# Kernel optimization log

Measured on AMD Instinct MI355X. Metric: run time of the kernel, lower is better.

The kernel has to match this reference:

```python
import jax, jax.numpy as jnp
import numpy as np

N_NODES = 50000
N_EDGES = 800000
D_FEAT = 128      # node feature dim (== coef_dim)
COEF_DIM = 128
OUT_DIM = 128     # node_layer / neighbour_layer output dim
EPS = 1e-12       # tf.math.l2_normalize epsilon


def setup_inputs() -> dict:
    key = jax.random.key(0)
    ks = jax.random.split(key, 8)
    s = 1.0 / np.sqrt(D_FEAT)
    h = jax.random.normal(ks[0], (N_NODES, D_FEAT), dtype=jnp.float32)
    src = jax.random.randint(ks[1], (N_EDGES,), 0, N_NODES, dtype=jnp.int32)
    dst = jax.random.randint(ks[2], (N_EDGES,), 0, N_NODES, dtype=jnp.int32)
    W_coef = jax.random.normal(ks[3], (D_FEAT, COEF_DIM), dtype=jnp.float32) * s
    b_coef = jnp.zeros((COEF_DIM,), dtype=jnp.float32)
    W_red = jax.random.normal(ks[4], (2 * COEF_DIM, 1), dtype=jnp.float32) * (1.0 / np.sqrt(2 * COEF_DIM))
    b_red = jnp.zeros((1,), dtype=jnp.float32)
    W_node = jax.random.normal(ks[5], (D_FEAT, OUT_DIM), dtype=jnp.float32) * s
    b_node = jnp.zeros((OUT_DIM,), dtype=jnp.float32)
    W_neigh = jax.random.normal(ks[6], (D_FEAT, OUT_DIM), dtype=jnp.float32) * s
    b_neigh = jnp.zeros((OUT_DIM,), dtype=jnp.float32)
    return {"h": h, "src": src, "dst": dst,
            "W_coef": W_coef, "b_coef": b_coef,
            "W_red": W_red, "b_red": b_red,
            "W_node": W_node, "b_node": b_node,
            "W_neigh": W_neigh, "b_neigh": b_neigh}


def reference(h, src, dst, W_coef, b_coef, W_red, b_red, W_node, b_node, W_neigh, b_neigh):
    n = h.shape[0]
    # message func: per-edge coef transform of source features (activation=None)
    q = h @ W_coef + b_coef                      # [N, C] dst-side coef features
    m = q[src]                                   # [E, C] (coef_layer(h[src]))
    # reduce func: attention score per edge from concat(dst coef, message)
    e = jnp.concatenate([q[dst], m], axis=-1) @ W_red + b_red   # [E, 1]
    e = e[:, 0]
    # softmax over incoming edges of each destination node (stable)
    emax = jax.ops.segment_max(e, dst, num_segments=n)          # [N]
    ex = jnp.exp(e - emax[dst])                                 # [E]
    denom = jax.ops.segment_sum(ex, dst, num_segments=n)        # [N]
    alpha = ex / (denom[dst] + EPS)                             # [E]
    # weighted neighbour aggregation of raw source features ('neigh' mailbox)
    agg = jax.ops.segment_sum(alpha[:, None] * h[src], dst, num_segments=n)  # [N, D]
    # new_h = concat(node_layer(h), neighbour_layer(agg))
    new_h = jnp.concatenate([h @ W_node + b_node, agg @ W_neigh + b_neigh], axis=-1)  # [N, 2*OUT]
    # tf.math.l2_normalize along last axis
    sq = jnp.sum(new_h * new_h, axis=-1, keepdims=True)
    return new_h * jax.lax.rsqrt(jnp.maximum(sq, EPS))
```

## Files before the change

### kernel.cpp

```cpp
#include <hip/hip_runtime.h>
#include <hip/hip_bf16.h>
#include <math.h>

#define N_NODES 50000
#define N_EDGES 800000
#define D_FEAT  128
#define EPSF    1e-12f

#define NPG     120
#define NG      417
#define CHUNK_E 4096
#define NCHUNK  196
#define GCAP    2560

#define OFF_U2      0
#define OFF_GCUR    1024
#define OFF_ES      4096
#define OFF_ROWPTR  204800
#define OFF_WTN     405504
#define OFF_WTG     438272
#define OFF_SSRCW   471040
#define OFF_HB      6871040
#define OFF_BUCKET  19671040

typedef __attribute__((ext_vector_type(8))) short bf8;
typedef __attribute__((ext_vector_type(4))) float f4;

__global__ void make_u2_kernel(const float* __restrict__ W_coef,
                               const float* __restrict__ W_red,
                               float* __restrict__ u2, int* __restrict__ gcursor) {
    __shared__ float wr[128];
    int k = threadIdx.x;
    wr[k] = W_red[128 + k];
    for (int i = k; i < NG; i += 128) gcursor[i] = 0;
    __syncthreads();
    const float4* row = (const float4*)(W_coef + k * 128);
    float acc = 0.f;
    #pragma unroll
    for (int j = 0; j < 32; ++j) {
        float4 v = row[j];
        acc += v.x * wr[4*j] + v.y * wr[4*j+1] + v.z * wr[4*j+2] + v.w * wr[4*j+3];
    }
    u2[k] = acc;
}

__global__ __launch_bounds__(256) void prep_kernel(
        const float* __restrict__ h, const float* __restrict__ u2,
        const float* __restrict__ Wn, const float* __restrict__ Wg,
        const int* __restrict__ src, const int* __restrict__ dst,
        float* __restrict__ es, unsigned short* __restrict__ hb,
        unsigned short* __restrict__ WtN, unsigned short* __restrict__ WtG,
        int* __restrict__ gcursor, int* __restrict__ bucket) {
    int b = blockIdx.x;
    if (b < 12500) {
        int node = b * 4 + (threadIdx.x >> 6);
        int lane = threadIdx.x & 63;
        float2 hv = ((const float2*)(h + (size_t)node * 128))[lane];
        float2 uv = ((const float2*)u2)[lane];
        float v = hv.x * uv.x + hv.y * uv.y;
        #pragma unroll
        for (int off = 32; off; off >>= 1) v += __shfl_xor(v, off);
        if (lane == 0) es[node] = __expf(v);
        __hip_bfloat162 p = __float22bfloat162_rn(hv);
        ((unsigned int*)(hb + (size_t)node * 128))[lane] = *(unsigned int*)&p;
    } else if (b < 12564) {
        int idx = (b - 12500) * 256 + threadIdx.x;
        int n = idx >> 7, k = idx & 127;
        __hip_bfloat16 a = __float2bfloat16(Wn[k * 128 + n]);
        __hip_bfloat16 g = __float2bfloat16(Wg[k * 128 + n]);
        WtN[n * 128 + k] = *(unsigned short*)&a;
        WtG[n * 128 + k] = *(unsigned short*)&g;
    } else {
        __shared__ int lh[NG];
        __shared__ int base[NG];
        __shared__ int cnt2[NG];
        int chunk = b - 12564;
        int tid = threadIdx.x;
        for (int i = tid; i < NG; i += 256) { lh[i] = 0; cnt2[i] = 0; }
        __syncthreads();
        int base_e = chunk * CHUNK_E;
        #pragma unroll
        for (int it = 0; it < CHUNK_E / 256; ++it) {
            int e = base_e + it * 256 + tid;
            if (e < N_EDGES) atomicAdd(&lh[(unsigned)dst[e] / NPG], 1);
        }
        __syncthreads();
        for (int i = tid; i < NG; i += 256) {
            int c = lh[i];
            base[i] = c ? atomicAdd(&gcursor[i], c) : 0;
        }
        __syncthreads();
        #pragma unroll
        for (int it = 0; it < CHUNK_E / 256; ++it) {
            int e = base_e + it * 256 + tid;
            if (e < N_EDGES) {
                int d = dst[e];
                int g = (unsigned)d / NPG;
                int r = atomicAdd(&cnt2[g], 1);
                int p = base[g] + r;
                if (p < GCAP)
                    bucket[(size_t)g * GCAP + p] = src[e] | ((d - g * NPG) << 16);
            }
        }
    }
}

__global__ __launch_bounds__(128) void fine_kernel(
        const int* __restrict__ gcnt, const int* __restrict__ bucket,
        const float* __restrict__ es,
        int* __restrict__ row_ptr, int2* __restrict__ ssrc_w) {
    __shared__ int cnt[NPG];
    __shared__ int cnt2[NPG];
    __shared__ int sexcl[NPG];
    __shared__ int ws[2];
    __shared__ int red[2];
    int g = blockIdx.x, tid = threadIdx.x;
    int lane = tid & 63, wid = tid >> 6;

    int partial = 0;
    for (int i = tid; i < g; i += 128) partial += gcnt[i];
    #pragma unroll
    for (int off = 32; off; off >>= 1) partial += __shfl_down(partial, off);
    if (lane == 0) red[wid] = partial;
    if (tid < NPG) { cnt[tid] = 0; cnt2[tid] = 0; }
    __syncthreads();
    int beg = red[0] + red[1];
    int cnt_g = min(gcnt[g], GCAP);
    const int* bk = bucket + (size_t)g * GCAP;

    for (int i = tid; i < cnt_g; i += 128)
        atomicAdd(&cnt[bk[i] >> 16], 1);
    __syncthreads();
    int v = (tid < NPG) ? cnt[tid] : 0;
    int incl = v;
    #pragma unroll
    for (int off = 1; off < 64; off <<= 1) {
        int t = __shfl_up(incl, off);
        if (lane >= off) incl += t;
    }
    if (lane == 63) ws[wid] = incl;
    __syncthreads();
    if (wid == 1) incl += ws[0];
    int excl = incl - v;
    if (tid < NPG) sexcl[tid] = excl;
    int node = g * NPG + tid;
    if (tid < NPG && node < N_NODES) row_ptr[node] = beg + excl;
    if (g == NG - 1 && tid == 0) row_ptr[N_NODES] = N_EDGES;
    __syncthreads();
    for (int i = tid; i < cnt_g; i += 128) {
        int p = bk[i];
        int loc = p >> 16;
        int sv = p & 0xFFFF;
        float wv = es[sv];
        int r = atomicAdd(&cnt2[loc], 1);
        ssrc_w[beg + sexcl[loc] + r] = make_int2(sv, __float_as_int(wv));
    }
}

__global__ __launch_bounds__(512) void agg_gemm_kernel(
        const int* __restrict__ row_ptr, const int2* __restrict__ ssrc_w,
        const unsigned short* __restrict__ hb,
        const unsigned short* __restrict__ WtN, const unsigned short* __restrict__ WtG,
        const float* __restrict__ b_node, const float* __restrict__ b_neigh,
        float* __restrict__ out) {
    __shared__ __align__(16) unsigned short aggt[32][136];
    __shared__ float ssrp[8][16];
    int tid = threadIdx.x;
    int wave = tid >> 6, lane = tid & 63;
    int node0 = blockIdx.x * 32;
    int q = lane >> 4, l16 = lane & 15;

    {
        int g32 = tid >> 4;
        int node = node0 + g32;
        int beg = 0, deg = 0;
        if (node < N_NODES) {
            beg = row_ptr[node];
            deg = row_ptr[node + 1] - beg;
        }
        float acc[8] = {0.f, 0.f, 0.f, 0.f, 0.f, 0.f, 0.f, 0.f};
        float wsum = 0.f;
        #pragma unroll 4
        for (int i = 0; i < deg; ++i) {
            int2 pw = ssrc_w[beg + i];
            float wv = __int_as_float(pw.y);
            wsum += wv;
            uint4 hv = *(const uint4*)(hb + (size_t)pw.x * 128 + l16 * 8);
            acc[0] = fmaf(wv, __uint_as_float(hv.x << 16),        acc[0]);
            acc[1] = fmaf(wv, __uint_as_float(hv.x & 0xFFFF0000u), acc[1]);
            acc[2] = fmaf(wv, __uint_as_float(hv.y << 16),        acc[2]);
            acc[3] = fmaf(wv, __uint_as_float(hv.y & 0xFFFF0000u), acc[3]);
            acc[4] = fmaf(wv, __uint_as_float(hv.z << 16),        acc[4]);
            acc[5] = fmaf(wv, __uint_as_float(hv.z & 0xFFFF0000u), acc[5]);
            acc[6] = fmaf(wv, __uint_as_float(hv.w << 16),        acc[6]);
            acc[7] = fmaf(wv, __uint_as_float(hv.w & 0xFFFF0000u), acc[7]);
        }
        float inv = 1.f / (wsum + EPSF);
        unsigned o[4];
        #pragma unroll
        for (int j = 0; j < 4; ++j) {
            __hip_bfloat162 p = __float22bfloat162_rn(
                make_float2(acc[2*j] * inv, acc[2*j+1] * inv));
            o[j] = *(unsigned*)&p;
        }
        *(uint4*)&aggt[g32][l16 * 8] = make_uint4(o[0], o[1], o[2], o[3]);
    }
    __syncthreads();

    int rt = wave & 1, tq = wave >> 1;
    int half = tq >> 1, tb = (tq & 1) * 4;
    const unsigned short* Wt = half ? WtG : WtN;
    size_t arow = (size_t)min(node0 + rt * 16 + l16, N_NODES - 1);

    f4 acc[4];
    #pragma unroll
    for (int tt = 0; tt < 4; ++tt) acc[tt] = (f4){0.f, 0.f, 0.f, 0.f};
    #pragma unroll
    for (int kc = 0; kc < 4; ++kc) {
        int kbase = kc * 32 + q * 8;
        bf8 a = half ? *(const bf8*)&aggt[rt * 16 + l16][kbase]
                     : *(const bf8*)(hb + arow * 128 + kbase);
        #pragma unroll
        for (int tt = 0; tt < 4; ++tt) {
            int t = tb + tt;
            bf8 bb = *(const bf8*)(Wt + (size_t)(t * 16 + l16) * 128 + kbase);
            acc[tt] = __builtin_amdgcn_mfma_f32_16x16x32_bf16(a, bb, acc[tt], 0, 0, 0);
        }
    }

    float ssr[4] = {0.f, 0.f, 0.f, 0.f};
    #pragma unroll
    for (int tt = 0; tt < 4; ++tt) {
        int t = tb + tt;
        float bv = (half ? b_neigh : b_node)[t * 16 + l16];
        #pragma unroll
        for (int r = 0; r < 4; ++r) {
            acc[tt][r] += bv;
            ssr[r] = fmaf(acc[tt][r], acc[tt][r], ssr[r]);
        }
    }
    #pragma unroll
    for (int r = 0; r < 4; ++r) {
        ssr[r] += __shfl_xor(ssr[r], 1);
        ssr[r] += __shfl_xor(ssr[r], 2);
        ssr[r] += __shfl_xor(ssr[r], 4);
        ssr[r] += __shfl_xor(ssr[r], 8);
    }
    if (l16 == 0) {
        #pragma unroll
        for (int r = 0; r < 4; ++r) ssrp[wave][q * 4 + r] = ssr[r];
    }
    __syncthreads();
    #pragma unroll
    for (int r = 0; r < 4; ++r) {
        int row = q * 4 + r;
        float tot = ssrp[rt][row] + ssrp[rt + 2][row] +
                    ssrp[rt + 4][row] + ssrp[rt + 6][row];
        float sc = rsqrtf(fmaxf(tot, EPSF));
        int node = node0 + rt * 16 + row;
        if (node < N_NODES) {
            float* o = out + (size_t)node * 256 + half * 128;
            #pragma unroll
            for (int tt = 0; tt < 4; ++tt)
                o[(tb + tt) * 16 + l16] = acc[tt][r] * sc;
        }
    }
}

extern "C" void kernel_launch(void* const* d_in, const int* in_sizes, int n_in,
                              void* d_out, int out_size, void* d_ws, size_t ws_size,
                              hipStream_t stream) {
    const float* h       = (const float*)d_in[0];
    const int*   src     = (const int*)d_in[1];
    const int*   dst     = (const int*)d_in[2];
    const float* W_coef  = (const float*)d_in[3];
    const float* W_red   = (const float*)d_in[5];
    const float* W_node  = (const float*)d_in[7];
    const float* b_node  = (const float*)d_in[8];
    const float* W_neigh = (const float*)d_in[9];
    const float* b_neigh = (const float*)d_in[10];
    float* out = (float*)d_out;

    char* w = (char*)d_ws;
    float*          u2      = (float*)(w + OFF_U2);
    int*            gcursor = (int*)(w + OFF_GCUR);
    float*          es      = (float*)(w + OFF_ES);
    int*            row_ptr = (int*)(w + OFF_ROWPTR);
    unsigned short* WtN     = (unsigned short*)(w + OFF_WTN);
    unsigned short* WtG     = (unsigned short*)(w + OFF_WTG);
    int2*           ssrc_w  = (int2*)(w + OFF_SSRCW);
    unsigned short* hb      = (unsigned short*)(w + OFF_HB);
    int*            bucket  = (int*)(w + OFF_BUCKET);

    make_u2_kernel<<<1, 128, 0, stream>>>(W_coef, W_red, u2, gcursor);
    prep_kernel<<<12500 + 64 + NCHUNK, 256, 0, stream>>>(
        h, u2, W_node, W_neigh, src, dst, es, hb, WtN, WtG, gcursor, bucket);
    fine_kernel<<<NG, 128, 0, stream>>>(gcursor, bucket, es, row_ptr, ssrc_w);
    agg_gemm_kernel<<<(N_NODES + 31) / 32, 512, 0, stream>>>(
        row_ptr, ssrc_w, hb, WtN, WtG, b_node, b_neigh, out);
}
```

Measured before the change: 198.6 us.

## Fuse fine CSR sort into aggregation kernel using per-block LDS edge lists

Removes the separate fine_kernel that built a global CSR (row_ptr, ssrc_w). Each aggregation block now re-reads its 128-node bucket, filters the edges for its 32 nodes, and builds a local edge list in shared memory with a count and scan. Groups become powers of two so shifts replace divisions. Each 256-thread block handles two nodes per 16-lane group and gives each wave all 8 output tiles. This saves a launch and a global write and read pass, but each bucket is scanned four times and SBCAP could overflow on high-degree subgroups.

New measurement: 210.6 us. 6.1% more time.

```diff
diff --git a/kernel.cpp b/kernel.cpp
--- a/kernel.cpp
+++ b/kernel.cpp
@@ -7,21 +7,20 @@
 #define D_FEAT  128
 #define EPSF    1e-12f
 
-#define NPG     120
-#define NG      417
+#define NPG     128
+#define NG      391
 #define CHUNK_E 4096
 #define NCHUNK  196
 #define GCAP    2560
+#define SBCAP   768
 
 #define OFF_U2      0
 #define OFF_GCUR    1024
 #define OFF_ES      4096
-#define OFF_ROWPTR  204800
-#define OFF_WTN     405504
-#define OFF_WTG     438272
-#define OFF_SSRCW   471040
-#define OFF_HB      6871040
-#define OFF_BUCKET  19671040
+#define OFF_WTN     204800
+#define OFF_WTG     237568
+#define OFF_HB      270336
+#define OFF_BUCKET  13070336
 
 typedef __attribute__((ext_vector_type(8))) short bf8;
 typedef __attribute__((ext_vector_type(4))) float f4;
@@ -82,7 +81,7 @@
         #pragma unroll
         for (int it = 0; it < CHUNK_E / 256; ++it) {
             int e = base_e + it * 256 + tid;
-            if (e < N_EDGES) atomicAdd(&lh[(unsigned)dst[e] / NPG], 1);
+            if (e < N_EDGES) atomicAdd(&lh[(unsigned)dst[e] >> 7], 1);
         }
         __syncthreads();
         for (int i = tid; i < NG; i += 256) {
@@ -95,97 +94,96 @@
             int e = base_e + it * 256 + tid;
             if (e < N_EDGES) {
                 int d = dst[e];
-                int g = (unsigned)d / NPG;
+                int g = (unsigned)d >> 7;
                 int r = atomicAdd(&cnt2[g], 1);
                 int p = base[g] + r;
                 if (p < GCAP)
-                    bucket[(size_t)g * GCAP + p] = src[e] | ((d - g * NPG) << 16);
+                    bucket[(size_t)g * GCAP + p] = src[e] | ((d & 127) << 16);
             }
         }
     }
 }
 
-__global__ __launch_bounds__(128) void fine_kernel(
+__global__ __launch_bounds__(256, 6) void agg_gemm_kernel(
         const int* __restrict__ gcnt, const int* __restrict__ bucket,
-        const float* __restrict__ es,
-        int* __restrict__ row_ptr, int2* __restrict__ ssrc_w) {
-    __shared__ int cnt[NPG];
-    __shared__ int cnt2[NPG];
-    __shared__ int sexcl[NPG];
-    __shared__ int ws[2];
-    __shared__ int red[2];
-    int g = blockIdx.x, tid = threadIdx.x;
-    int lane = tid & 63, wid = tid >> 6;
-
-    int partial = 0;
-    for (int i = tid; i < g; i += 128) partial += gcnt[i];
-    #pragma unroll
-    for (int off = 32; off; off >>= 1) partial += __shfl_down(partial, off);
-    if (lane == 0) red[wid] = partial;
-    if (tid < NPG) { cnt[tid] = 0; cnt2[tid] = 0; }
-    __syncthreads();
-    int beg = red[0] + red[1];
-    int cnt_g = min(gcnt[g], GCAP);
-    const int* bk = bucket + (size_t)g * GCAP;
-
-    for (int i = tid; i < cnt_g; i += 128)
-        atomicAdd(&cnt[bk[i] >> 16], 1);
-    __syncthreads();
-    int v = (tid < NPG) ? cnt[tid] : 0;
-    int incl = v;
-    #pragma unroll
-    for (int off = 1; off < 64; off <<= 1) {
-        int t = __shfl_up(incl, off);
-        if (lane >= off) incl += t;
-    }
-    if (lane == 63) ws[wid] = incl;
-    __syncthreads();
-    if (wid == 1) incl += ws[0];
-    int excl = incl - v;
-    if (tid < NPG) sexcl[tid] = excl;
-    int node = g * NPG + tid;
-    if (tid < NPG && node < N_NODES) row_ptr[node] = beg + excl;
-    if (g == NG - 1 && tid == 0) row_ptr[N_NODES] = N_EDGES;
-    __syncthreads();
-    for (int i = tid; i < cnt_g; i += 128) {
-        int p = bk[i];
-        int loc = p >> 16;
-        int sv = p & 0xFFFF;
-        float wv = es[sv];
-        int r = atomicAdd(&cnt2[loc], 1);
-        ssrc_w[beg + sexcl[loc] + r] = make_int2(sv, __float_as_int(wv));
-    }
-}
-
-__global__ __launch_bounds__(512) void agg_gemm_kernel(
-        const int* __restrict__ row_ptr, const int2* __restrict__ ssrc_w,
-        const unsigned short* __restrict__ hb,
+        const float* __restrict__ es, const unsigned short* __restrict__ hb,
         const unsigned short* __restrict__ WtN, const unsigned short* __restrict__ WtG,
         const float* __restrict__ b_node, const float* __restrict__ b_neigh,
         float* __restrict__ out) {
+    __shared__ int cnt[32];
+    __shared__ int nbeg[33];
+    __shared__ int cur[32];
+    __shared__ __align__(8) int2 elist[SBCAP];
     __shared__ __align__(16) unsigned short aggt[32][136];
-    __shared__ float ssrp[8][16];
+    __shared__ float ssrp[4][16];
     int tid = threadIdx.x;
-    int wave = tid >> 6, lane = tid & 63;
-    int node0 = blockIdx.x * 32;
-    int q = lane >> 4, l16 = lane & 15;
+    int g = blockIdx.x >> 2, sb = blockIdx.x & 3;
+    int node0 = g * NPG + sb * 32;
+    if (node0 >= N_NODES) return;
+
+    if (tid < 32) cnt[tid] = 0;
+    __syncthreads();
+
+    int cnt_g = min(gcnt[g], GCAP);
+    const int* bk = bucket + (size_t)g * GCAP;
+
+    for (int i = tid; i < cnt_g; i += 256) {
+        int loc = bk[i] >> 16;
+        if ((loc >> 5) == sb) atomicAdd(&cnt[loc & 31], 1);
+    }
+    __syncthreads();
+    if (tid < 64) {
+        int v = (tid < 32) ? cnt[tid] : 0;
+        int incl = v;
+        #pragma unroll
+        for (int off = 1; off < 32; off <<= 1) {
+            int t = __shfl_up(incl, off);
+            if (tid >= off) incl += t;
+        }
+        if (tid < 32) { nbeg[tid] = incl - v; cur[tid] = incl - v; }
+        if (tid == 31) nbeg[32] = incl;
+    }
+    __syncthreads();
+    for (int i = tid; i < cnt_g; i += 256) {
+        int p = bk[i];
+        int loc = p >> 16;
+        if ((loc >> 5) == sb) {
+            int sv = p & 0xFFFF;
+            int r = atomicAdd(&cur[loc & 31], 1);
+            if (r < SBCAP) elist[r] = make_int2(sv, __float_as_int(es[sv]));
+        }
+    }
+    __syncthreads();
 
     {
-        int g32 = tid >> 4;
-        int node = node0 + g32;
-        int beg = 0, deg = 0;
-        if (node < N_NODES) {
-            beg = row_ptr[node];
-            deg = row_ptr[node + 1] - beg;
-        }
+        int q = tid >> 4, l16 = tid & 15;
+        int a = nbeg[2 * q], m = nbeg[2 * q + 1], b2 = nbeg[2 * q + 2];
         float acc[8] = {0.f, 0.f, 0.f, 0.f, 0.f, 0.f, 0.f, 0.f};
         float wsum = 0.f;
-        #pragma unroll 4
-        for (int i = 0; i < deg; ++i) {
-            int2 pw = ssrc_w[beg + i];
-            float wv = __int_as_float(pw.y);
+        int currow = 2 * q;
+        auto flush = [&](int row) {
+            float inv = 1.f / (wsum + EPSF);
+            unsigned o[4];
+            #pragma unroll
+            for (int j = 0; j < 4; ++j) {
+                __hip_bfloat162 pk = __float22bfloat162_rn(
+                    make_float2(acc[2*j] * inv, acc[2*j+1] * inv));
+                o[j] = *(unsigned*)&pk;
+            }
+            *(uint4*)&aggt[row][l16 * 8] = make_uint4(o[0], o[1], o[2], o[3]);
+        };
+        for (int i = a; i < b2; ++i) {
+            if (i == m) {
+                flush(currow);
+                #pragma unroll
+                for (int j = 0; j < 8; ++j) acc[j] = 0.f;
+                wsum = 0.f;
+                currow = 2 * q + 1;
+            }
+            int2 e = elist[i];
+            float wv = __int_as_float(e.y);
             wsum += wv;
-            uint4 hv = *(const uint4*)(hb + (size_t)pw.x * 128 + l16 * 8);
+            uint4 hv = *(const uint4*)(hb + (size_t)e.x * 128 + l16 * 8);
             acc[0] = fmaf(wv, __uint_as_float(hv.x << 16),        acc[0]);
             acc[1] = fmaf(wv, __uint_as_float(hv.x & 0xFFFF0000u), acc[1]);
             acc[2] = fmaf(wv, __uint_as_float(hv.y << 16),        acc[2]);
@@ -195,48 +193,47 @@
             acc[6] = fmaf(wv, __uint_as_float(hv.w << 16),        acc[6]);
             acc[7] = fmaf(wv, __uint_as_float(hv.w & 0xFFFF0000u), acc[7]);
         }
-        float inv = 1.f / (wsum + EPSF);
-        unsigned o[4];
-        #pragma unroll
-        for (int j = 0; j < 4; ++j) {
-            __hip_bfloat162 p = __float22bfloat162_rn(
-                make_float2(acc[2*j] * inv, acc[2*j+1] * inv));
-            o[j] = *(unsigned*)&p;
-        }
-        *(uint4*)&aggt[g32][l16 * 8] = make_uint4(o[0], o[1], o[2], o[3]);
-    }
-    __syncthreads();
-
-    int rt = wave & 1, tq = wave >> 1;
-    int half = tq >> 1, tb = (tq & 1) * 4;
+        flush(currow);
+        if (currow == 2 * q) {
+            #pragma unroll
+            for (int j = 0; j < 8; ++j) acc[j] = 0.f;
+            wsum = 0.f;
+            flush(2 * q + 1);
+        }
+    }
+    __syncthreads();
+
+    int wave = tid >> 6, lane = tid & 63;
+    int q4 = lane >> 4, l16 = lane & 15;
+    int rt = wave & 1, half = wave >> 1;
     const unsigned short* Wt = half ? WtG : WtN;
-    size_t arow = (size_t)min(node0 + rt * 16 + l16, N_NODES - 1);
-
-    f4 acc[4];
-    #pragma unroll
-    for (int tt = 0; tt < 4; ++tt) acc[tt] = (f4){0.f, 0.f, 0.f, 0.f};
+    int lrow = rt * 16 + l16;
+    size_t arow = (size_t)min(node0 + lrow, N_NODES - 1);
+
+    f4 acc8[8];
+    #pragma unroll
+    for (int t = 0; t < 8; ++t) acc8[t] = (f4){0.f, 0.f, 0.f, 0.f};
     #pragma unroll
     for (int kc = 0; kc < 4; ++kc) {
-        int kbase = kc * 32 + q * 8;
-        bf8 a = half ? *(const bf8*)&aggt[rt * 16 + l16][kbase]
+        int kbase = kc * 32 + q4 * 8;
+        bf8 a = half ? *(const bf8*)&aggt[lrow][kbase]
                      : *(const bf8*)(hb + arow * 128 + kbase);
         #pragma unroll
-        for (int tt = 0; tt < 4; ++tt) {
-            int t = tb + tt;
+        for (int t = 0; t < 8; ++t) {
             bf8 bb = *(const bf8*)(Wt + (size_t)(t * 16 + l16) * 128 + kbase);
-            acc[tt] = __builtin_amdgcn_mfma_f32_16x16x32_bf16(a, bb, acc[tt], 0, 0, 0);
-        }
-    }
-
+            acc8[t] = __builtin_amdgcn_mfma_f32_16x16x32_bf16(a, bb, acc8[t], 0, 0, 0);
+        }
+    }
+
+    const float* bias = half ? b_neigh : b_node;
     float ssr[4] = {0.f, 0.f, 0.f, 0.f};
     #pragma unroll
-    for (int tt = 0; tt < 4; ++tt) {
-        int t = tb + tt;
-        float bv = (half ? b_neigh : b_node)[t * 16 + l16];
+    for (int t = 0; t < 8; ++t) {
+        float bv = bias[t * 16 + l16];
         #pragma unroll
         for (int r = 0; r < 4; ++r) {
-            acc[tt][r] += bv;
-            ssr[r] = fmaf(acc[tt][r], acc[tt][r], ssr[r]);
+            acc8[t][r] += bv;
+            ssr[r] = fmaf(acc8[t][r], acc8[t][r], ssr[r]);
         }
     }
     #pragma unroll
@@ -248,21 +245,20 @@
     }
     if (l16 == 0) {
         #pragma unroll
-        for (int r = 0; r < 4; ++r) ssrp[wave][q * 4 + r] = ssr[r];
+        for (int r = 0; r < 4; ++r) ssrp[wave][q4 * 4 + r] = ssr[r];
     }
     __syncthreads();
     #pragma unroll
     for (int r = 0; r < 4; ++r) {
-        int row = q * 4 + r;
-        float tot = ssrp[rt][row] + ssrp[rt + 2][row] +
-                    ssrp[rt + 4][row] + ssrp[rt + 6][row];
+        int rowin = q4 * 4 + r;
+        float tot = ssrp[rt][rowin] + ssrp[rt + 2][rowin];
         float sc = rsqrtf(fmaxf(tot, EPSF));
-        int node = node0 + rt * 16 + row;
+        int node = node0 + rt * 16 + rowin;
         if (node < N_NODES) {
             float* o = out + (size_t)node * 256 + half * 128;
             #pragma unroll
-            for (int tt = 0; tt < 4; ++tt)
-                o[(tb + tt) * 16 + l16] = acc[tt][r] * sc;
+            for (int t = 0; t < 8; ++t)
+                o[t * 16 + l16] = acc8[t][r] * sc;
         }
     }
 }
@@ -285,17 +281,14 @@
     float*          u2      = (float*)(w + OFF_U2);
     int*            gcursor = (int*)(w + OFF_GCUR);
     float*          es      = (float*)(w + OFF_ES);
-    int*            row_ptr = (int*)(w + OFF_ROWPTR);
     unsigned short* WtN     = (unsigned short*)(w + OFF_WTN);
     unsigned short* WtG     = (unsigned short*)(w + OFF_WTG);
-    int2*           ssrc_w  = (int2*)(w + OFF_SSRCW);
     unsigned short* hb      = (unsigned short*)(w + OFF_HB);
     int*            bucket  = (int*)(w + OFF_BUCKET);
 
     make_u2_kernel<<<1, 128, 0, stream>>>(W_coef, W_red, u2, gcursor);
     prep_kernel<<<12500 + 64 + NCHUNK, 256, 0, stream>>>(
         h, u2, W_node, W_neigh, src, dst, es, hb, WtN, WtG, gcursor, bucket);
-    fine_kernel<<<NG, 128, 0, stream>>>(gcursor, bucket, es, row_ptr, ssrc_w);
-    agg_gemm_kernel<<<(N_NODES + 31) / 32, 512, 0, stream>>>(
-        row_ptr, ssrc_w, hb, WtN, WtG, b_node, b_neigh, out);
-}
+    agg_gemm_kernel<<<NG * 4, 256, 0, stream>>>(
+        gcursor, bucket, es, hb, WtN, WtG, b_node, b_neigh, out);
+}
```

## Stage block edge list in LDS and gather features in four narrow passes

Applied to the files above, without the earlier changes.

The aggregation step now copies each block's contiguous edge list (up to 768 entries) into shared memory once, then makes four passes over the edges. Each pass gathers 4 bytes per lane covering a 32-column slice, where before each lane loaded 16 bytes per edge. The aim is to cut per-thread register pressure and fix the gather access pattern, but edge reads now happen four times from LDS and the number of gather load instructions rises. The sorting chunk size is also halved, with the chunk count doubled to match.

Result: slower. 243.4 us (+22.6%).

```diff
diff --git a/kernel.cpp b/kernel.cpp
--- a/kernel.cpp
+++ b/kernel.cpp
@@ -9,9 +9,10 @@
 
 #define NPG     120
 #define NG      417
-#define CHUNK_E 4096
-#define NCHUNK  196
+#define CHUNK_E 2048
+#define NCHUNK  391
 #define GCAP    2560
+#define ELCAP   768
 
 #define OFF_U2      0
 #define OFF_GCUR    1024
@@ -163,12 +164,19 @@
         const unsigned short* __restrict__ WtN, const unsigned short* __restrict__ WtG,
         const float* __restrict__ b_node, const float* __restrict__ b_neigh,
         float* __restrict__ out) {
+    __shared__ __align__(8) int2 el[ELCAP];
     __shared__ __align__(16) unsigned short aggt[32][136];
     __shared__ float ssrp[8][16];
     int tid = threadIdx.x;
     int wave = tid >> 6, lane = tid & 63;
     int node0 = blockIdx.x * 32;
     int q = lane >> 4, l16 = lane & 15;
+
+    int ebeg = row_ptr[min(node0, N_NODES)];
+    int eend = row_ptr[min(node0 + 32, N_NODES)];
+    int ecnt = eend - ebeg;
+    for (int i = tid; i < min(ecnt, ELCAP); i += 512) el[i] = ssrc_w[ebeg + i];
+    __syncthreads();
 
     {
         int g32 = tid >> 4;
@@ -178,32 +186,39 @@
             beg = row_ptr[node];
             deg = row_ptr[node + 1] - beg;
         }
-        float acc[8] = {0.f, 0.f, 0.f, 0.f, 0.f, 0.f, 0.f, 0.f};
-        float wsum = 0.f;
-        #pragma unroll 4
-        for (int i = 0; i < deg; ++i) {
-            int2 pw = ssrc_w[beg + i];
-            float wv = __int_as_float(pw.y);
-            wsum += wv;
-            uint4 hv = *(const uint4*)(hb + (size_t)pw.x * 128 + l16 * 8);
-            acc[0] = fmaf(wv, __uint_as_float(hv.x << 16),        acc[0]);
-            acc[1] = fmaf(wv, __uint_as_float(hv.x & 0xFFFF0000u), acc[1]);
-            acc[2] = fmaf(wv, __uint_as_float(hv.y << 16),        acc[2]);
-            acc[3] = fmaf(wv, __uint_as_float(hv.y & 0xFFFF0000u), acc[3]);
-            acc[4] = fmaf(wv, __uint_as_float(hv.z << 16),        acc[4]);
-            acc[5] = fmaf(wv, __uint_as_float(hv.z & 0xFFFF0000u), acc[5]);
-            acc[6] = fmaf(wv, __uint_as_float(hv.w << 16),        acc[6]);
-            acc[7] = fmaf(wv, __uint_as_float(hv.w & 0xFFFF0000u), acc[7]);
-        }
-        float inv = 1.f / (wsum + EPSF);
-        unsigned o[4];
-        #pragma unroll
-        for (int j = 0; j < 4; ++j) {
-            __hip_bfloat162 p = __float22bfloat162_rn(
-                make_float2(acc[2*j] * inv, acc[2*j+1] * inv));
-            o[j] = *(unsigned*)&p;
-        }
-        *(uint4*)&aggt[g32][l16 * 8] = make_uint4(o[0], o[1], o[2], o[3]);
+        int rbeg = beg - ebeg;
+        float inv;
+        {
+            float a0 = 0.f, a1 = 0.f, wsum = 0.f;
+            #pragma unroll 4
+            for (int i = 0; i < deg; ++i) {
+                int ri = rbeg + i;
+                int2 pw = (ri < ELCAP) ? el[ri] : ssrc_w[beg + i];
+                float wv = __int_as_float(pw.y);
+                wsum += wv;
+                unsigned hv = *(const unsigned*)(hb + (size_t)pw.x * 128 + l16 * 2);
+                a0 = fmaf(wv, __uint_as_float(hv << 16),         a0);
+                a1 = fmaf(wv, __uint_as_float(hv & 0xFFFF0000u), a1);
+            }
+            inv = 1.f / (wsum + EPSF);
+            __hip_bfloat162 p = __float22bfloat162_rn(make_float2(a0 * inv, a1 * inv));
+            *(unsigned*)&aggt[g32][l16 * 2] = *(unsigned*)&p;
+        }
+        #pragma unroll
+        for (int ks = 1; ks < 4; ++ks) {
+            float a0 = 0.f, a1 = 0.f;
+            #pragma unroll 4
+            for (int i = 0; i < deg; ++i) {
+                int ri = rbeg + i;
+                int2 pw = (ri < ELCAP) ? el[ri] : ssrc_w[beg + i];
+                float wv = __int_as_float(pw.y);
+                unsigned hv = *(const unsigned*)(hb + (size_t)pw.x * 128 + ks * 32 + l16 * 2);
+                a0 = fmaf(wv, __uint_as_float(hv << 16),         a0);
+                a1 = fmaf(wv, __uint_as_float(hv & 0xFFFF0000u), a1);
+            }
+            __hip_bfloat162 p = __float22bfloat162_rn(make_float2(a0 * inv, a1 * inv));
+            *(unsigned*)&aggt[g32][ks * 32 + l16 * 2] = *(unsigned*)&p;
+        }
     }
     __syncthreads();
 
```
